# Performance work log

Hardware: AMD Instinct MI355X
Metric: run time of the kernel (lower is better)

## Reference

```python
import jax, jax.numpy as jnp
import numpy as np

EMBED_DIM = 2048
NUM_HEADS = 32
NUM_KV_HEADS = 8
HEAD_DIM = EMBED_DIM // NUM_HEADS
KV_REPEAT = NUM_HEADS // NUM_KV_HEADS
ROPE_BASE = 10000.0


def rotate_half(x):
    # interleaved rotate: (-x_odd, x_even) re-interleaved on last dim
    x_even = x[..., ::2]
    x_odd = x[..., 1::2]
    return jnp.stack((-x_odd, x_even), axis=-1).reshape(x.shape)


def rope_cos_sin(seq_len, dtype, start_pos=0):
    inv_freq = 1.0 / (ROPE_BASE ** (jnp.arange(0, HEAD_DIM, 2, dtype=jnp.float32) / HEAD_DIM))
    pos = jnp.arange(start_pos, start_pos + seq_len, dtype=jnp.float32)
    freqs = jnp.outer(pos, inv_freq)  # [T, head_dim/2]
    cos = jnp.repeat(jnp.cos(freqs), 2, axis=-1).astype(dtype)  # [T, head_dim]
    sin = jnp.repeat(jnp.sin(freqs), 2, axis=-1).astype(dtype)
    return cos[None, None], sin[None, None]  # [1,1,T,head_dim]


def setup_inputs() -> dict:
    key = jax.random.key(0)
    ks = jax.random.split(key, 5)
    s = 0.02
    x = jax.random.normal(ks[0], (2, 2048, EMBED_DIM), dtype=jnp.float32)
    Wq = jax.random.normal(ks[1], (EMBED_DIM, EMBED_DIM), dtype=jnp.float32) * s
    Wk = jax.random.normal(ks[2], (EMBED_DIM, NUM_KV_HEADS * HEAD_DIM), dtype=jnp.float32) * s
    Wv = jax.random.normal(ks[3], (EMBED_DIM, NUM_KV_HEADS * HEAD_DIM), dtype=jnp.float32) * s
    Wo = jax.random.normal(ks[4], (EMBED_DIM, EMBED_DIM), dtype=jnp.float32) * s
    return {
        "x": x,
        "Wq": Wq, "bq": jnp.zeros((EMBED_DIM,), jnp.float32),
        "Wk": Wk, "bk": jnp.zeros((NUM_KV_HEADS * HEAD_DIM,), jnp.float32),
        "Wv": Wv, "bv": jnp.zeros((NUM_KV_HEADS * HEAD_DIM,), jnp.float32),
        "Wo": Wo, "bo": jnp.zeros((EMBED_DIM,), jnp.float32),
    }


def reference(x, Wq, bq, Wk, bk, Wv, bv, Wo, bo):
    B, T, C = x.shape
    q = (x @ Wq + bq).reshape(B, T, NUM_HEADS, HEAD_DIM).transpose(0, 2, 1, 3)      # [B,H,T,D]
    k = (x @ Wk + bk).reshape(B, T, NUM_KV_HEADS, HEAD_DIM).transpose(0, 2, 1, 3)   # [B,Hkv,T,D]
    v = (x @ Wv + bv).reshape(B, T, NUM_KV_HEADS, HEAD_DIM).transpose(0, 2, 1, 3)

    cos, sin = rope_cos_sin(T, q.dtype, start_pos=0)
    q = q * cos + rotate_half(q) * sin
    k = k * cos + rotate_half(k) * sin

    # GQA: repeat KV heads to match query heads (faithful to repeat_interleave)
    k_rep = jnp.repeat(k, KV_REPEAT, axis=1)  # [B,H,T,D]
    v_rep = jnp.repeat(v, KV_REPEAT, axis=1)

    scale = np.sqrt(HEAD_DIM).astype(np.float32)
    scores = jnp.einsum('bhqd,bhkd->bhqk', q, k_rep) / scale  # [B,H,T,T]

    # causal mask: key_pos > query_pos -> -inf
    qpos = jnp.arange(T)[:, None]
    kpos = jnp.arange(T)[None, :]
    scores = jnp.where((kpos > qpos)[None, None], -jnp.inf, scores)

    attn = jax.nn.softmax(scores, axis=-1)
    out = jnp.einsum('bhqk,bhkd->bhqd', attn, v_rep)  # [B,H,T,D]
    out = out.transpose(0, 2, 1, 3).reshape(B, T, C)
    return out @ Wo + bo
```

## Files before the change

### kernel.cpp

```cpp
#include <hip/hip_runtime.h>
#include <hip/hip_bf16.h>
#include <stdint.h>
#include <stddef.h>

#define EMBED 2048
#define TLEN  2048
#define BSZ   2
#define NH    32
#define NKV   8
#define HD    64
#define MROWS (BSZ*TLEN)
#define KVD   (NKV*HD)
#define QKVN  3072

typedef __attribute__((ext_vector_type(8))) short   s16x8;
typedef __attribute__((ext_vector_type(4))) short   s16x4;
typedef __attribute__((ext_vector_type(8))) __bf16  bf16x8;
typedef __attribute__((ext_vector_type(4))) float   f32x4;
typedef __attribute__((ext_vector_type(2))) unsigned long long u64x2;
typedef __attribute__((ext_vector_type(4))) uint32_t u32x4;

static __device__ __forceinline__ float bf2f(short u) {
  union { float f; uint32_t i; } c; c.i = ((uint32_t)(uint16_t)u) << 16; return c.f;
}
static __device__ __forceinline__ short f2bf(float f) {
  union { float f; uint32_t i; } c; c.f = f;
  uint32_t x = c.i;
  uint32_t r = (x + 0x7fffu + ((x >> 16) & 1u)) >> 16;
  return (short)(uint16_t)r;
}
static __device__ __forceinline__ bf16x8 as_bf16x8(s16x8 s) {
  return __builtin_bit_cast(bf16x8, s);
}
static __device__ __forceinline__ bf16x8 mk8(unsigned long long a, unsigned long long b) {
  u64x2 t; t.x = a; t.y = b;
  return __builtin_bit_cast(bf16x8, t);
}
static __device__ __forceinline__ bf16x8 mk8w(uint32_t w0, uint32_t w1,
                                              uint32_t w2, uint32_t w3) {
  u32x4 t; t.x = w0; t.y = w1; t.z = w2; t.w = w3;
  return __builtin_bit_cast(bf16x8, t);
}

__global__ __launch_bounds__(256) void transpose_cast_kernel(
    const float* __restrict__ W, short* __restrict__ Wt, int K, int N) {
  __shared__ float tile[32][33];
  int n0 = blockIdx.x * 32, k0 = blockIdx.y * 32;
  int tx = threadIdx.x, ty = threadIdx.y;
  #pragma unroll
  for (int i = 0; i < 32; i += 8)
    tile[ty + i][tx] = W[(size_t)(k0 + ty + i) * N + n0 + tx];
  __syncthreads();
  #pragma unroll
  for (int i = 0; i < 32; i += 8)
    Wt[(size_t)(n0 + ty + i) * K + k0 + tx] = f2bf(tile[tx][ty + i]);
}

__global__ __launch_bounds__(256) void cast_bf16_kernel(
    const float* __restrict__ in, short* __restrict__ out, int n) {
  int i = (blockIdx.x * blockDim.x + threadIdx.x) * 4;
  if (i >= n) return;
  f32x4 v = *(const f32x4*)(in + i);
  s16x4 o = { f2bf(v.x), f2bf(v.y), f2bf(v.z), f2bf(v.w) };
  *(s16x4*)(out + i) = o;
}

template<bool OUT_F32, bool TRIPLE_BIAS>
__global__ __launch_bounds__(256) void gemm_bt(
    const short* __restrict__ A, const short* __restrict__ Bt,
    const float* __restrict__ b0, const float* __restrict__ b1,
    const float* __restrict__ b2, void* __restrict__ Cout, int ldc) {
  const int K = 2048;
  __shared__ __align__(16) short As[128 * 32];
  __shared__ __align__(16) short Bs[128 * 32];
  int bn = blockIdx.x, bm = blockIdx.y;
  int tid = threadIdx.x;
  int lane = tid & 63, wave = tid >> 6;
  int wr = wave >> 1, wc = wave & 1;
  int fr = lane & 15, fk = lane >> 4;
  f32x4 acc[4][4] = {};
  const short* Ab = A + (size_t)bm * 128 * K;
  const short* Bb = Bt + (size_t)bn * 128 * K;
  for (int kt = 0; kt < K; kt += 32) {
    #pragma unroll
    for (int ii = 0; ii < 2; ++ii) {
      const int i = wave * 2 + ii;
      const int r = i * 16 + (lane >> 2);
      const int c = lane & 3;
      const size_t go = (size_t)r * K + kt + c * 8;
      __builtin_amdgcn_global_load_lds(
          (const __attribute__((address_space(1))) void*)(Ab + go),
          (__attribute__((address_space(3))) void*)&As[i * 512], 16, 0, 0);
      __builtin_amdgcn_global_load_lds(
          (const __attribute__((address_space(1))) void*)(Bb + go),
          (__attribute__((address_space(3))) void*)&Bs[i * 512], 16, 0, 0);
    }
    __syncthreads();
    bf16x8 af[4], bfr[4];
    #pragma unroll
    for (int m = 0; m < 4; ++m)
      af[m] = as_bf16x8(*(const s16x8*)&As[(wr * 64 + m * 16 + fr) * 32 + fk * 8]);
    #pragma unroll
    for (int n = 0; n < 4; ++n)
      bfr[n] = as_bf16x8(*(const s16x8*)&Bs[(wc * 64 + n * 16 + fr) * 32 + fk * 8]);
    __builtin_amdgcn_s_setprio(1);
    #pragma unroll
    for (int m = 0; m < 4; ++m)
      #pragma unroll
      for (int n = 0; n < 4; ++n)
        acc[m][n] = __builtin_amdgcn_mfma_f32_16x16x32_bf16(af[m], bfr[n], acc[m][n], 0, 0, 0);
    __builtin_amdgcn_s_setprio(0);
    __syncthreads();
  }
  int row0 = bm * 128 + wr * 64;
  int col0 = bn * 128 + wc * 64;
  #pragma unroll
  for (int n = 0; n < 4; ++n) {
    int col = col0 + n * 16 + fr;
    float bv;
    if constexpr (TRIPLE_BIAS)
      bv = (col < 2048) ? b0[col] : ((col < 2560) ? b1[col - 2048] : b2[col - 2560]);
    else
      bv = b0[col];
    #pragma unroll
    for (int m = 0; m < 4; ++m)
      #pragma unroll
      for (int j = 0; j < 4; ++j) {
        int row = row0 + m * 16 + fk * 4 + j;
        float v = acc[m][n][j] + bv;
        if constexpr (OUT_F32) ((float*)Cout)[(size_t)row * ldc + col] = v;
        else                   ((short*)Cout)[(size_t)row * ldc + col] = f2bf(v);
      }
  }
}

__global__ __launch_bounds__(256) void rope_table_kernel(float2* __restrict__ tab) {
  int idx = blockIdx.x * 256 + threadIdx.x;
  int t = idx >> 5, i = idx & 31;
  float ang = (float)t * powf(10000.0f, -(float)i / 32.0f);
  float c, s;
  sincosf(ang, &c, &s);
  tab[idx] = make_float2(c, s);
}

__global__ __launch_bounds__(256) void rope_apply_kernel(
    short* __restrict__ X, int ncols, int ldx, float oscale,
    const float2* __restrict__ tab) {
  int idx = blockIdx.x * 256 + threadIdx.x;
  int npr = ncols >> 1;
  int row = idx / npr, cp = idx - row * npr;
  int i = cp & 31;
  int t = row & (TLEN - 1);
  float2 cs = tab[(t << 5) | i];
  short* p = X + (size_t)row * ldx + cp * 2;
  float e = bf2f(p[0]), o = bf2f(p[1]);
  p[0] = f2bf((e * cs.x + o * cs.y) * oscale);
  p[1] = f2bf((o * cs.x - e * cs.y) * oscale);
}

__global__ __launch_bounds__(256) void attn_kernel(
    const short* __restrict__ Q, const short* __restrict__ Kx,
    const short* __restrict__ Vx, short* __restrict__ O) {
  const int pr = blockIdx.x;
  const int bh = blockIdx.y;
  const int b = bh >> 5, h = bh & 31, kvh = h >> 2;
  const int tid = threadIdx.x;
  const int lane = tid & 63, wave = tid >> 6;
  const int fr = lane & 15, fk = lane >> 4;

  __shared__ __align__(16) short Ks[64][72];
  __shared__ __align__(16) short VS[4 * 1040];

  const short* Kbase = Kx + (size_t)b * TLEN * QKVN + kvh * HD;
  const short* Vbase = Vx + (size_t)b * TLEN * QKVN + kvh * HD;

  const int srow = tid >> 3;
  const int scb  = (tid & 7) << 3;
  const int vd0  = scb >> 4;
  const int vco  = scb & 15;
  const int p0 = (((srow >> 2) & 3) << 3) | (((srow >> 4) & 1) << 2) | (srow & 3);
  const int vaddr0 = vd0 * 1040 + ((p0 >> 2) << 6) + ((p0 & 3) << 4) + vco;
  const int vaddr1 = vaddr0 + 512;
  const unsigned trb = (unsigned)(unsigned long long)&VS[fk * 128 + fr * 4];
  const bf16x8 ones = mk8(0x3F803F803F803F80ULL, 0x3F803F803F803F80ULL);

#define TRREAD(dst, OFF) asm volatile("ds_read_b64_tr_b16 %0, %1 offset:" OFF \
    : "=v"(dst) : "v"(trb) : "memory")
#define CVTPK(d, lo, hi) asm volatile("v_cvt_pk_bf16_f32 %0, %1, %2" \
    : "=v"(d) : "v"(lo), "v"(hi))

  #pragma unroll 1
  for (int rep = 0; rep < 2; ++rep) {
    const int qt = rep ? (31 - pr) : pr;
    const int q0 = qt * 64;
    const short* Qrow = Q + (size_t)(b * TLEN + q0 + wave * 16 + fr) * QKVN + h * HD;
    const bf16x8 aq0 = as_bf16x8(*(const s16x8*)&Qrow[fk * 8]);
    const bf16x8 aq1 = as_bf16x8(*(const s16x8*)&Qrow[32 + fk * 8]);
    f32x4 oacc[4] = {};
    f32x4 lacc = {};
    float m = -INFINITY;
    const int qloc = wave * 16 + fr;

    for (int kv0 = 0; kv0 <= q0; kv0 += 64) {
      #pragma unroll
      for (int it = 0; it < 2; ++it) {
        const int r = srow + it * 32;
        const size_t gro = (size_t)(kv0 + r) * QKVN + scb;
        *(s16x8*)&Ks[r][scb] = *(const s16x8*)&Kbase[gro];
        s16x8 vv = *(const s16x8*)&Vbase[gro];
        *(s16x8*)&VS[it ? vaddr1 : vaddr0] = vv;
      }
      __syncthreads();

      f32x4 sacc[4] = {};
      {
        bf16x8 bk0[4], bk1[4];
        #pragma unroll
        for (int mb = 0; mb < 4; ++mb) {
          bk0[mb] = as_bf16x8(*(const s16x8*)&Ks[mb * 16 + fr][fk * 8]);
          bk1[mb] = as_bf16x8(*(const s16x8*)&Ks[mb * 16 + fr][32 + fk * 8]);
        }
        __builtin_amdgcn_s_setprio(1);
        #pragma unroll
        for (int mb = 0; mb < 4; ++mb) {
          sacc[mb] = __builtin_amdgcn_mfma_f32_16x16x32_bf16(bk0[mb], aq0, sacc[mb], 0, 0, 0);
          sacc[mb] = __builtin_amdgcn_mfma_f32_16x16x32_bf16(bk1[mb], aq1, sacc[mb], 0, 0, 0);
        }
        __builtin_amdgcn_s_setprio(0);
      }

      const bool diag = (kv0 == q0);
      float sv[4][4];
      float pm = -INFINITY;
      #pragma unroll
      for (int mb = 0; mb < 4; ++mb)
        #pragma unroll
        for (int j = 0; j < 4; ++j) {
          float v = sacc[mb][j];
          if (diag && (mb * 16 + fk * 4 + j > qloc)) v = -INFINITY;
          sv[mb][j] = v;
          pm = fmaxf(pm, v);
        }
      pm = fmaxf(pm, __shfl_xor(pm, 16, 64));
      pm = fmaxf(pm, __shfl_xor(pm, 32, 64));

      if (__any(pm > m + 11.5f)) {
        const float mnew = fmaxf(m, pm);
        const float al = exp2f(m - mnew);
        m = mnew;
        lacc[0] *= al; lacc[1] *= al; lacc[2] *= al; lacc[3] *= al;
        #pragma unroll
        for (int db = 0; db < 4; ++db) {
          oacc[db][0] *= al; oacc[db][1] *= al;
          oacc[db][2] *= al; oacc[db][3] *= al;
        }
      }

      uint32_t rlo[4], rhi[4];
      #pragma unroll
      for (int mb = 0; mb < 4; ++mb) {
        float e0 = exp2f(sv[mb][0] - m);
        float e1 = exp2f(sv[mb][1] - m);
        float e2 = exp2f(sv[mb][2] - m);
        float e3 = exp2f(sv[mb][3] - m);
        CVTPK(rlo[mb], e0, e1);
        CVTPK(rhi[mb], e2, e3);
      }
      const bf16x8 pB0 = mk8w(rlo[0], rhi[0], rlo[1], rhi[1]);
      const bf16x8 pB1 = mk8w(rlo[2], rhi[2], rlo[3], rhi[3]);

      unsigned long long t00, t01, t02, t03, t10, t11, t12, t13;
      unsigned long long t20, t21, t22, t23, t30, t31, t32, t33;
      TRREAD(t00, "0");    TRREAD(t01, "128");  TRREAD(t02, "1024"); TRREAD(t03, "1152");
      TRREAD(t10, "2080"); TRREAD(t11, "2208"); TRREAD(t12, "3104"); TRREAD(t13, "3232");
      TRREAD(t20, "4160"); TRREAD(t21, "4288"); TRREAD(t22, "5184"); TRREAD(t23, "5312");
      TRREAD(t30, "6240"); TRREAD(t31, "6368"); TRREAD(t32, "7264"); TRREAD(t33, "7392");
      asm volatile("s_waitcnt lgkmcnt(0)" ::: "memory");
      __builtin_amdgcn_sched_barrier(0);
      __builtin_amdgcn_s_setprio(1);
      lacc = __builtin_amdgcn_mfma_f32_16x16x32_bf16(ones, pB0, lacc, 0, 0, 0);
      lacc = __builtin_amdgcn_mfma_f32_16x16x32_bf16(ones, pB1, lacc, 0, 0, 0);
      oacc[0] = __builtin_amdgcn_mfma_f32_16x16x32_bf16(mk8(t00, t01), pB0, oacc[0], 0, 0, 0);
      oacc[0] = __builtin_amdgcn_mfma_f32_16x16x32_bf16(mk8(t02, t03), pB1, oacc[0], 0, 0, 0);
      oacc[1] = __builtin_amdgcn_mfma_f32_16x16x32_bf16(mk8(t10, t11), pB0, oacc[1], 0, 0, 0);
      oacc[1] = __builtin_amdgcn_mfma_f32_16x16x32_bf16(mk8(t12, t13), pB1, oacc[1], 0, 0, 0);
      oacc[2] = __builtin_amdgcn_mfma_f32_16x16x32_bf16(mk8(t20, t21), pB0, oacc[2], 0, 0, 0);
      oacc[2] = __builtin_amdgcn_mfma_f32_16x16x32_bf16(mk8(t22, t23), pB1, oacc[2], 0, 0, 0);
      oacc[3] = __builtin_amdgcn_mfma_f32_16x16x32_bf16(mk8(t30, t31), pB0, oacc[3], 0, 0, 0);
      oacc[3] = __builtin_amdgcn_mfma_f32_16x16x32_bf16(mk8(t32, t33), pB1, oacc[3], 0, 0, 0);
      __builtin_amdgcn_s_setprio(0);
      __syncthreads();
    }

    {
      const float linv = 1.0f / lacc[0];
      short* orow = O + (size_t)(b * TLEN + q0 + wave * 16 + fr) * EMBED + h * HD + fk * 4;
      #pragma unroll
      for (int db = 0; db < 4; ++db) {
        s16x4 o4 = { f2bf(oacc[db][0] * linv), f2bf(oacc[db][1] * linv),
                     f2bf(oacc[db][2] * linv), f2bf(oacc[db][3] * linv) };
        *(s16x4*)&orow[db * 16] = o4;
      }
    }
  }
#undef TRREAD
#undef CVTPK
}

extern "C" void kernel_launch(void* const* d_in, const int* in_sizes, int n_in,
                              void* d_out, int out_size, void* d_ws, size_t ws_size,
                              hipStream_t stream) {
  const float* x  = (const float*)d_in[0];
  const float* Wq = (const float*)d_in[1];
  const float* bq = (const float*)d_in[2];
  const float* Wk = (const float*)d_in[3];
  const float* bk = (const float*)d_in[4];
  const float* Wv = (const float*)d_in[5];
  const float* bv = (const float*)d_in[6];
  const float* Wo = (const float*)d_in[7];
  const float* bo = (const float*)d_in[8];
  float* out = (float*)d_out;

  char* ws = (char*)d_ws;
  short* xb    = (short*)(ws);
  short* WqkvT = (short*)(ws + 16777216);
  short* WoT   = (short*)(ws + 29360128);
  short* QKV   = (short*)(ws + 37748736);
  short* Ob    = (short*)(ws);
  float2* tab  = (float2*)d_out;

  dim3 tb(32, 8);
  transpose_cast_kernel<<<dim3(EMBED / 32, EMBED / 32), tb, 0, stream>>>(Wq, WqkvT, EMBED, EMBED);
  transpose_cast_kernel<<<dim3(KVD / 32, EMBED / 32), tb, 0, stream>>>(Wk, WqkvT + (size_t)2048 * 2048, EMBED, KVD);
  transpose_cast_kernel<<<dim3(KVD / 32, EMBED / 32), tb, 0, stream>>>(Wv, WqkvT + (size_t)2560 * 2048, EMBED, KVD);
  transpose_cast_kernel<<<dim3(EMBED / 32, EMBED / 32), tb, 0, stream>>>(Wo, WoT, EMBED, EMBED);
  cast_bf16_kernel<<<(MROWS * EMBED / 4) / 256, 256, 0, stream>>>(x, xb, MROWS * EMBED);
  rope_table_kernel<<<256, 256, 0, stream>>>(tab);

  gemm_bt<false, true><<<dim3(QKVN / 128, MROWS / 128), 256, 0, stream>>>(
      xb, WqkvT, bq, bk, bv, QKV, QKVN);

  rope_apply_kernel<<<(MROWS * (EMBED / 2)) / 256, 256, 0, stream>>>(
      QKV, EMBED, QKVN, 0.125f * 1.44269504088896340736f, tab);
  rope_apply_kernel<<<(MROWS * (KVD / 2)) / 256, 256, 0, stream>>>(
      QKV + 2048, KVD, QKVN, 1.0f, tab);

  attn_kernel<<<dim3(16, BSZ * NH), 256, 0, stream>>>(
      QKV, QKV + 2048, QKV + 2560, Ob);

  gemm_bt<true, false><<<dim3(EMBED / 128, MROWS / 128), 256, 0, stream>>>(
      Ob, WoT, bo, bo, bo, out, EMBED);
}
```

Before: 242.6 us.

## Fuse RoPE into QKV GEMM epilogue, swizzle GEMM blocks, widen attention KV tile

Moves RoPE and the Q scale into the QKV GEMM epilogue, using a lane shuffle to fetch each pair partner, and drops the two standalone rope kernels and their extra read/write passes over Q and K. Adds an XCD-style block-index swizzle to both GEMMs to improve L2 locality. The attention kernel now processes 128 keys per iteration instead of 64, halving barrier and loop overhead, at the cost of more shared memory and registers, plus extra masked work on the last diagonal tile.

```diff
diff --git a/kernel.cpp b/kernel.cpp
--- a/kernel.cpp
+++ b/kernel.cpp
@@ -65,15 +65,28 @@
   *(s16x4*)(out + i) = o;
 }
 
-template<bool OUT_F32, bool TRIPLE_BIAS>
+__global__ __launch_bounds__(256) void rope_table_kernel(float2* __restrict__ tab) {
+  int idx = blockIdx.x * 256 + threadIdx.x;
+  int t = idx >> 5, i = idx & 31;
+  float ang = (float)t * powf(10000.0f, -(float)i / 32.0f);
+  float c, s;
+  sincosf(ang, &c, &s);
+  tab[idx] = make_float2(c, s);
+}
+
+template<bool OUT_F32, bool TRIPLE_BIAS, bool ROPE>
 __global__ __launch_bounds__(256) void gemm_bt(
     const short* __restrict__ A, const short* __restrict__ Bt,
     const float* __restrict__ b0, const float* __restrict__ b1,
-    const float* __restrict__ b2, void* __restrict__ Cout, int ldc) {
+    const float* __restrict__ b2, void* __restrict__ Cout, int ldc,
+    const float2* __restrict__ tab) {
   const int K = 2048;
   __shared__ __align__(16) short As[128 * 32];
   __shared__ __align__(16) short Bs[128 * 32];
-  int bn = blockIdx.x, bm = blockIdx.y;
+  int flat = blockIdx.y * gridDim.x + blockIdx.x;
+  int cpx = (gridDim.x * gridDim.y) >> 3;
+  int swz = (flat & 7) * cpx + (flat >> 3);
+  int bn = swz % gridDim.x, bm = swz / gridDim.x;
   int tid = threadIdx.x;
   int lane = tid & 63, wave = tid >> 6;
   int wr = wave >> 1, wc = wave & 1;
@@ -114,6 +127,7 @@
   }
   int row0 = bm * 128 + wr * 64;
   int col0 = bn * 128 + wc * 64;
+  const float QSC = 0.125f * 1.44269504088896340736f;
   #pragma unroll
   for (int n = 0; n < 4; ++n) {
     int col = col0 + n * 16 + fr;
@@ -122,40 +136,26 @@
       bv = (col < 2048) ? b0[col] : ((col < 2560) ? b1[col - 2048] : b2[col - 2560]);
     else
       bv = b0[col];
+    const bool dorope = ROPE && (col < 2560);
+    const float sc = (col < 2048) ? QSC : 1.0f;
+    const int ci = (col & 63) >> 1;
+    const bool even = (fr & 1) == 0;
     #pragma unroll
     for (int m = 0; m < 4; ++m)
       #pragma unroll
       for (int j = 0; j < 4; ++j) {
         int row = row0 + m * 16 + fk * 4 + j;
         float v = acc[m][n][j] + bv;
+        if (dorope) {
+          const int t = row & (TLEN - 1);
+          const float2 cs = tab[(t << 5) | ci];
+          const float p = __shfl_xor(v, 1, 64);
+          v = (even ? (v * cs.x + p * cs.y) : (v * cs.x - p * cs.y)) * sc;
+        }
         if constexpr (OUT_F32) ((float*)Cout)[(size_t)row * ldc + col] = v;
         else                   ((short*)Cout)[(size_t)row * ldc + col] = f2bf(v);
       }
   }
-}
-
-__global__ __launch_bounds__(256) void rope_table_kernel(float2* __restrict__ tab) {
-  int idx = blockIdx.x * 256 + threadIdx.x;
-  int t = idx >> 5, i = idx & 31;
-  float ang = (float)t * powf(10000.0f, -(float)i / 32.0f);
-  float c, s;
-  sincosf(ang, &c, &s);
-  tab[idx] = make_float2(c, s);
-}
-
-__global__ __launch_bounds__(256) void rope_apply_kernel(
-    short* __restrict__ X, int ncols, int ldx, float oscale,
-    const float2* __restrict__ tab) {
-  int idx = blockIdx.x * 256 + threadIdx.x;
-  int npr = ncols >> 1;
-  int row = idx / npr, cp = idx - row * npr;
-  int i = cp & 31;
-  int t = row & (TLEN - 1);
-  float2 cs = tab[(t << 5) | i];
-  short* p = X + (size_t)row * ldx + cp * 2;
-  float e = bf2f(p[0]), o = bf2f(p[1]);
-  p[0] = f2bf((e * cs.x + o * cs.y) * oscale);
-  p[1] = f2bf((o * cs.x - e * cs.y) * oscale);
 }
 
 __global__ __launch_bounds__(256) void attn_kernel(
@@ -168,8 +168,8 @@
   const int lane = tid & 63, wave = tid >> 6;
   const int fr = lane & 15, fk = lane >> 4;
 
-  __shared__ __align__(16) short Ks[64][72];
-  __shared__ __align__(16) short VS[4 * 1040];
+  __shared__ __align__(16) short Ks[128][72];
+  __shared__ __align__(16) short VS[2 * 4160];
 
   const short* Kbase = Kx + (size_t)b * TLEN * QKVN + kvh * HD;
   const short* Vbase = Vx + (size_t)b * TLEN * QKVN + kvh * HD;
@@ -179,15 +179,42 @@
   const int vd0  = scb >> 4;
   const int vco  = scb & 15;
   const int p0 = (((srow >> 2) & 3) << 3) | (((srow >> 4) & 1) << 2) | (srow & 3);
-  const int vaddr0 = vd0 * 1040 + ((p0 >> 2) << 6) + ((p0 & 3) << 4) + vco;
-  const int vaddr1 = vaddr0 + 512;
-  const unsigned trb = (unsigned)(unsigned long long)&VS[fk * 128 + fr * 4];
+  const int vbase0 = vd0 * 1040 + ((p0 >> 2) << 6) + ((p0 & 3) << 4) + vco;
+  const int vbase1 = vbase0 + 512;
+  const unsigned trb0 = (unsigned)(unsigned long long)&VS[fk * 128 + fr * 4];
+  const unsigned trb1 = trb0 + 8320;
   const bf16x8 ones = mk8(0x3F803F803F803F80ULL, 0x3F803F803F803F80ULL);
 
-#define TRREAD(dst, OFF) asm volatile("ds_read_b64_tr_b16 %0, %1 offset:" OFF \
-    : "=v"(dst) : "v"(trb) : "memory")
+#define TRREAD(dst, BASE, OFF) asm volatile("ds_read_b64_tr_b16 %0, %1 offset:" OFF \
+    : "=v"(dst) : "v"(BASE) : "memory")
 #define CVTPK(d, lo, hi) asm volatile("v_cvt_pk_bf16_f32 %0, %1, %2" \
     : "=v"(d) : "v"(lo), "v"(hi))
+#define PVHALF(BASE, PA, PB) do { \
+  unsigned long long t00, t01, t02, t03, t10, t11, t12, t13; \
+  unsigned long long t20, t21, t22, t23, t30, t31, t32, t33; \
+  TRREAD(t00, BASE, "0");    TRREAD(t01, BASE, "128");  \
+  TRREAD(t02, BASE, "1024"); TRREAD(t03, BASE, "1152"); \
+  TRREAD(t10, BASE, "2080"); TRREAD(t11, BASE, "2208"); \
+  TRREAD(t12, BASE, "3104"); TRREAD(t13, BASE, "3232"); \
+  TRREAD(t20, BASE, "4160"); TRREAD(t21, BASE, "4288"); \
+  TRREAD(t22, BASE, "5184"); TRREAD(t23, BASE, "5312"); \
+  TRREAD(t30, BASE, "6240"); TRREAD(t31, BASE, "6368"); \
+  TRREAD(t32, BASE, "7264"); TRREAD(t33, BASE, "7392"); \
+  asm volatile("s_waitcnt lgkmcnt(0)" ::: "memory"); \
+  __builtin_amdgcn_sched_barrier(0); \
+  __builtin_amdgcn_s_setprio(1); \
+  lacc = __builtin_amdgcn_mfma_f32_16x16x32_bf16(ones, PA, lacc, 0, 0, 0); \
+  lacc = __builtin_amdgcn_mfma_f32_16x16x32_bf16(ones, PB, lacc, 0, 0, 0); \
+  oacc[0] = __builtin_amdgcn_mfma_f32_16x16x32_bf16(mk8(t00, t01), PA, oacc[0], 0, 0, 0); \
+  oacc[0] = __builtin_amdgcn_mfma_f32_16x16x32_bf16(mk8(t02, t03), PB, oacc[0], 0, 0, 0); \
+  oacc[1] = __builtin_amdgcn_mfma_f32_16x16x32_bf16(mk8(t10, t11), PA, oacc[1], 0, 0, 0); \
+  oacc[1] = __builtin_amdgcn_mfma_f32_16x16x32_bf16(mk8(t12, t13), PB, oacc[1], 0, 0, 0); \
+  oacc[2] = __builtin_amdgcn_mfma_f32_16x16x32_bf16(mk8(t20, t21), PA, oacc[2], 0, 0, 0); \
+  oacc[2] = __builtin_amdgcn_mfma_f32_16x16x32_bf16(mk8(t22, t23), PB, oacc[2], 0, 0, 0); \
+  oacc[3] = __builtin_amdgcn_mfma_f32_16x16x32_bf16(mk8(t30, t31), PA, oacc[3], 0, 0, 0); \
+  oacc[3] = __builtin_amdgcn_mfma_f32_16x16x32_bf16(mk8(t32, t33), PB, oacc[3], 0, 0, 0); \
+  __builtin_amdgcn_s_setprio(0); \
+} while (0)
 
   #pragma unroll 1
   for (int rep = 0; rep < 2; ++rep) {
@@ -201,44 +228,46 @@
     float m = -INFINITY;
     const int qloc = wave * 16 + fr;
 
-    for (int kv0 = 0; kv0 <= q0; kv0 += 64) {
-      #pragma unroll
-      for (int it = 0; it < 2; ++it) {
+    for (int kv0 = 0; kv0 < q0 + 64; kv0 += 128) {
+      #pragma unroll
+      for (int it = 0; it < 4; ++it) {
         const int r = srow + it * 32;
         const size_t gro = (size_t)(kv0 + r) * QKVN + scb;
         *(s16x8*)&Ks[r][scb] = *(const s16x8*)&Kbase[gro];
         s16x8 vv = *(const s16x8*)&Vbase[gro];
-        *(s16x8*)&VS[it ? vaddr1 : vaddr0] = vv;
+        *(s16x8*)&VS[(it >> 1) * 4160 + ((it & 1) ? vbase1 : vbase0)] = vv;
       }
       __syncthreads();
 
-      f32x4 sacc[4] = {};
-      {
-        bf16x8 bk0[4], bk1[4];
+      f32x4 sacc[8] = {};
+      #pragma unroll
+      for (int hf = 0; hf < 2; ++hf) {
+        bf16x8 k0[4], k1[4];
         #pragma unroll
         for (int mb = 0; mb < 4; ++mb) {
-          bk0[mb] = as_bf16x8(*(const s16x8*)&Ks[mb * 16 + fr][fk * 8]);
-          bk1[mb] = as_bf16x8(*(const s16x8*)&Ks[mb * 16 + fr][32 + fk * 8]);
+          const short* kr = &Ks[hf * 64 + mb * 16 + fr][0];
+          k0[mb] = as_bf16x8(*(const s16x8*)&kr[fk * 8]);
+          k1[mb] = as_bf16x8(*(const s16x8*)&kr[32 + fk * 8]);
         }
         __builtin_amdgcn_s_setprio(1);
         #pragma unroll
         for (int mb = 0; mb < 4; ++mb) {
-          sacc[mb] = __builtin_amdgcn_mfma_f32_16x16x32_bf16(bk0[mb], aq0, sacc[mb], 0, 0, 0);
-          sacc[mb] = __builtin_amdgcn_mfma_f32_16x16x32_bf16(bk1[mb], aq1, sacc[mb], 0, 0, 0);
+          sacc[hf * 4 + mb] = __builtin_amdgcn_mfma_f32_16x16x32_bf16(k0[mb], aq0, sacc[hf * 4 + mb], 0, 0, 0);
+          sacc[hf * 4 + mb] = __builtin_amdgcn_mfma_f32_16x16x32_bf16(k1[mb], aq1, sacc[hf * 4 + mb], 0, 0, 0);
         }
         __builtin_amdgcn_s_setprio(0);
       }
 
-      const bool diag = (kv0 == q0);
-      float sv[4][4];
+      const bool diag = (kv0 + 128 > q0);
+      const int thr = q0 + qloc - kv0;
       float pm = -INFINITY;
       #pragma unroll
-      for (int mb = 0; mb < 4; ++mb)
+      for (int mb = 0; mb < 8; ++mb)
         #pragma unroll
         for (int j = 0; j < 4; ++j) {
           float v = sacc[mb][j];
-          if (diag && (mb * 16 + fk * 4 + j > qloc)) v = -INFINITY;
-          sv[mb][j] = v;
+          if (diag && (mb * 16 + fk * 4 + j > thr)) v = -INFINITY;
+          sacc[mb][j] = v;
           pm = fmaxf(pm, v);
         }
       pm = fmaxf(pm, __shfl_xor(pm, 16, 64));
@@ -256,39 +285,23 @@
         }
       }
 
-      uint32_t rlo[4], rhi[4];
-      #pragma unroll
-      for (int mb = 0; mb < 4; ++mb) {
-        float e0 = exp2f(sv[mb][0] - m);
-        float e1 = exp2f(sv[mb][1] - m);
-        float e2 = exp2f(sv[mb][2] - m);
-        float e3 = exp2f(sv[mb][3] - m);
+      uint32_t rlo[8], rhi[8];
+      #pragma unroll
+      for (int mb = 0; mb < 8; ++mb) {
+        float e0 = exp2f(sacc[mb][0] - m);
+        float e1 = exp2f(sacc[mb][1] - m);
+        float e2 = exp2f(sacc[mb][2] - m);
+        float e3 = exp2f(sacc[mb][3] - m);
         CVTPK(rlo[mb], e0, e1);
         CVTPK(rhi[mb], e2, e3);
       }
       const bf16x8 pB0 = mk8w(rlo[0], rhi[0], rlo[1], rhi[1]);
       const bf16x8 pB1 = mk8w(rlo[2], rhi[2], rlo[3], rhi[3]);
-
-      unsigned long long t00, t01, t02, t03, t10, t11, t12, t13;
-      unsigned long long t20, t21, t22, t23, t30, t31, t32, t33;
-      TRREAD(t00, "0");    TRREAD(t01, "128");  TRREAD(t02, "1024"); TRREAD(t03, "1152");
-      TRREAD(t10, "2080"); TRREAD(t11, "2208"); TRREAD(t12, "3104"); TRREAD(t13, "3232");
-      TRREAD(t20, "4160"); TRREAD(t21, "4288"); TRREAD(t22, "5184"); TRREAD(t23, "5312");
-      TRREAD(t30, "6240"); TRREAD(t31, "6368"); TRREAD(t32, "7264"); TRREAD(t33, "7392");
-      asm volatile("s_waitcnt lgkmcnt(0)" ::: "memory");
-      __builtin_amdgcn_sched_barrier(0);
-      __builtin_amdgcn_s_setprio(1);
-      lacc = __builtin_amdgcn_mfma_f32_16x16x32_bf16(ones, pB0, lacc, 0, 0, 0);
-      lacc = __builtin_amdgcn_mfma_f32_16x16x32_bf16(ones, pB1, lacc, 0, 0, 0);
-      oacc[0] = __builtin_amdgcn_mfma_f32_16x16x32_bf16(mk8(t00, t01), pB0, oacc[0], 0, 0, 0);
-      oacc[0] = __builtin_amdgcn_mfma_f32_16x16x32_bf16(mk8(t02, t03), pB1, oacc[0], 0, 0, 0);
-      oacc[1] = __builtin_amdgcn_mfma_f32_16x16x32_bf16(mk8(t10, t11), pB0, oacc[1], 0, 0, 0);
-      oacc[1] = __builtin_amdgcn_mfma_f32_16x16x32_bf16(mk8(t12, t13), pB1, oacc[1], 0, 0, 0);
-      oacc[2] = __builtin_amdgcn_mfma_f32_16x16x32_bf16(mk8(t20, t21), pB0, oacc[2], 0, 0, 0);
-      oacc[2] = __builtin_amdgcn_mfma_f32_16x16x32_bf16(mk8(t22, t23), pB1, oacc[2], 0, 0, 0);
-      oacc[3] = __builtin_amdgcn_mfma_f32_16x16x32_bf16(mk8(t30, t31), pB0, oacc[3], 0, 0, 0);
-      oacc[3] = __builtin_amdgcn_mfma_f32_16x16x32_bf16(mk8(t32, t33), pB1, oacc[3], 0, 0, 0);
-      __builtin_amdgcn_s_setprio(0);
+      const bf16x8 pB2 = mk8w(rlo[4], rhi[4], rlo[5], rhi[5]);
+      const bf16x8 pB3 = mk8w(rlo[6], rhi[6], rlo[7], rhi[7]);
+
+      PVHALF(trb0, pB0, pB1);
+      PVHALF(trb1, pB2, pB3);
       __syncthreads();
     }
 
@@ -305,6 +318,7 @@
   }
 #undef TRREAD
 #undef CVTPK
+#undef PVHALF
 }
 
 extern "C" void kernel_launch(void* const* d_in, const int* in_sizes, int n_in,
@@ -337,17 +351,12 @@
   cast_bf16_kernel<<<(MROWS * EMBED / 4) / 256, 256, 0, stream>>>(x, xb, MROWS * EMBED);
   rope_table_kernel<<<256, 256, 0, stream>>>(tab);
 
-  gemm_bt<false, true><<<dim3(QKVN / 128, MROWS / 128), 256, 0, stream>>>(
-      xb, WqkvT, bq, bk, bv, QKV, QKVN);
-
-  rope_apply_kernel<<<(MROWS * (EMBED / 2)) / 256, 256, 0, stream>>>(
-      QKV, EMBED, QKVN, 0.125f * 1.44269504088896340736f, tab);
-  rope_apply_kernel<<<(MROWS * (KVD / 2)) / 256, 256, 0, stream>>>(
-      QKV + 2048, KVD, QKVN, 1.0f, tab);
+  gemm_bt<false, true, true><<<dim3(QKVN / 128, MROWS / 128), 256, 0, stream>>>(
+      xb, WqkvT, bq, bk, bv, QKV, QKVN, tab);
 
   attn_kernel<<<dim3(16, BSZ * NH), 256, 0, stream>>>(
       QKV, QKV + 2048, QKV + 2560, Ob);
 
-  gemm_bt<true, false><<<dim3(EMBED / 128, MROWS / 128), 256, 0, stream>>>(
-      Ob, WoT, bo, bo, bo, out, EMBED);
-}
+  gemm_bt<true, false, false><<<dim3(EMBED / 128, MROWS / 128), 256, 0, stream>>>(
+      Ob, WoT, bo, bo, bo, out, EMBED, tab);
+}
```

Measured after the change: 283.4 us. 1.17x slower.
